# Kernel tuning notes

Measured on AMD Instinct MI355X. Metric: run time of the kernel, lower is better.

Reference implementation:

```python
import jax, jax.numpy as jnp
import numpy as np

B, L, C = 32, 1024, 32     # batch, seq_len, enc_in
D = 512                     # d_model / hidden_size
SEG = 16                    # seg_len
K = 25                      # moving_avg kernel
SX = L // SEG               # seg_num_x = 64 sequential GRU steps
PRED = 16                   # pred_len == seg_len -> seg_num_y = 1


def setup_inputs() -> dict:
    key = jax.random.key(0)
    ks = jax.random.split(key, 20)
    r = lambda i, shape: jax.random.normal(ks[i], shape, dtype=jnp.float32) * 0.05
    return {
        "x": jax.random.normal(ks[0], (B, L, C), dtype=jnp.float32),
        "W_emb": r(1, (D, SEG)), "b_emb": r(2, (D,)),
        "Wih_s": r(3, (3 * D, D)), "Whh_s": r(4, (3 * D, D)),
        "bih_s": r(5, (3 * D,)), "bhh_s": r(6, (3 * D,)),
        "Wih_t": r(7, (3 * D, D)), "Whh_t": r(8, (3 * D, D)),
        "bih_t": r(9, (3 * D,)), "bhh_t": r(10, (3 * D,)),
        "pos_s": r(11, (1, D // 2)), "ch_s": r(12, (C, D // 2)),
        "pos_t": r(13, (1, D // 2)), "ch_t": r(14, (C, D // 2)),
        "Wps": r(15, (SEG, D)), "bps": r(16, (SEG,)),
        "Wpt": r(17, (SEG, D)), "bpt": r(18, (SEG,)),
    }


def _moving_mean(x, k):
    # Autoformer moving_avg over dim 1 with edge replication (length preserved, k odd)
    pad = (k - 1) // 2
    xp = jnp.concatenate([jnp.repeat(x[:, :1], pad, 1), x, jnp.repeat(x[:, -1:], pad, 1)], axis=1)
    cs = jnp.cumsum(xp, axis=1)
    cs = jnp.concatenate([jnp.zeros_like(cs[:, :1]), cs], axis=1)
    return (cs[:, k:] - cs[:, :-k]) / k


def _gru_cell(x, h, Wih, Whh, bih, bhh):
    gi = x @ Wih.T + bih
    gh = h @ Whh.T + bhh
    ir, iz, in_ = jnp.split(gi, 3, axis=-1)
    hr, hz, hn = jnp.split(gh, 3, axis=-1)
    r = jax.nn.sigmoid(ir + hr)
    z = jax.nn.sigmoid(iz + hz)
    n = jnp.tanh(in_ + r * hn)
    return (1.0 - z) * n + z * h


def _forward(x, W_emb, b_emb, Wih_s, Whh_s, bih_s, bhh_s, Wih_t, Whh_t, bih_t, bhh_t,
             pos_s, ch_s, pos_t, ch_t, Wps, bps, Wpt, bpt):
    seq_last = jax.lax.stop_gradient(x[:, -1:, :])          # (B,1,C), detached
    xc = (x - seq_last).transpose(0, 2, 1)                  # (B,C,L)
    mean = _moving_mean(xc, K)                              # trend
    xs = xc - mean                                          # seasonal residual
    xt = mean
    # value embedding: (B*C, SX, SEG) -> (B*C, SX, D), ReLU
    xs = jax.nn.relu(xs.reshape(-1, SX, SEG) @ W_emb.T + b_emb)
    xt = jax.nn.relu(xt.reshape(-1, SX, SEG) @ W_emb.T + b_emb)
    N = B * C
    h0 = jnp.zeros((N, D), x.dtype)

    def step(carry, inp):
        hs, ht = carry
        xs_i, xt_i = inp
        hs = _gru_cell(xs_i, hs, Wih_s, Whh_s, bih_s, bhh_s)
        ht = _gru_cell(xt_i, ht, Wih_t, Whh_t, bih_t, bhh_t)
        return (hs, ht), None

    (hs, ht), _ = jax.lax.scan(step, (h0, h0), (xs.transpose(1, 0, 2), xt.transpose(1, 0, 2)))

    # decoder (seg_num_y == 1): pos/channel embedding -> one more GRUCell step
    pe_s = jnp.tile(jnp.concatenate([jnp.broadcast_to(pos_s, (C, D // 2)), ch_s], -1), (B, 1))  # (B*C,D)
    pe_t = jnp.tile(jnp.concatenate([jnp.broadcast_to(pos_t, (C, D // 2)), ch_t], -1), (B, 1))
    hs2 = _gru_cell(pe_s, hs, Wih_s, Whh_s, bih_s, bhh_s)
    ht2 = _gru_cell(pe_t, ht, Wih_t, Whh_t, bih_t, bhh_t)
    # predict heads (dropout is identity in eval)
    y = ht2 @ Wpt.T + bpt + hs2 @ Wps.T + bps               # (B*C, SEG)
    y = y.reshape(B, C, PRED).transpose(0, 2, 1)            # (B, PRED, C)
    return y + seq_last


def reference(x, W_emb, b_emb, Wih_s, Whh_s, bih_s, bhh_s, Wih_t, Whh_t, bih_t, bhh_t,
              pos_s, ch_s, pos_t, ch_t, Wps, bps, Wpt, bpt):
    return _forward(x, W_emb, b_emb, Wih_s, Whh_s, bih_s, bhh_s, Wih_t, Whh_t, bih_t, bhh_t,
                    pos_s, ch_s, pos_t, ch_t, Wps, bps, Wpt, bpt)
```

## Files before the change

kernel.cpp:

```cpp
#include <hip/hip_runtime.h>
#include <math.h>

#define B_   32
#define L_   1024
#define C_   32
#define D_   512
#define SEG_ 16
#define SX_  64
#define N_   1024

typedef _Float16 f16x8 __attribute__((ext_vector_type(8)));
typedef _Float16 f16x4 __attribute__((ext_vector_type(4)));
typedef float    f32x4 __attribute__((ext_vector_type(4)));

__device__ __forceinline__ void stage16(const void* g, void* l) {
    __builtin_amdgcn_global_load_lds((const __attribute__((address_space(1))) void*)g,
                                     (__attribute__((address_space(3))) void*)l, 16, 0, 0);
}
__device__ __forceinline__ void stage16l(const void* g, void* l) {
    __builtin_amdgcn_global_load_lds((const __attribute__((address_space(1))) void*)g,
                                     (__attribute__((address_space(3))) void*)l, 16, 0, 1);
}
__device__ __forceinline__ void store_v4_sc0(void* p, f16x8 v) {
    asm volatile("global_store_dwordx4 %0, %1, off sc0" :: "v"(p), "v"(v) : "memory");
}
__device__ __forceinline__ float fsig(float x) {
    return __builtin_amdgcn_rcpf(1.f + __expf(-x));
}
__device__ __forceinline__ float ftanh(float x) {
    return 1.f - 2.f * __builtin_amdgcn_rcpf(1.f + __expf(2.f * x));
}

__global__ __launch_bounds__(256) void prep_kernel(const float* __restrict__ x,
                                                   float* __restrict__ xs_seg,
                                                   float* __restrict__ xt_seg) {
    int b = blockIdx.x >> 2;
    int t = ((blockIdx.x & 3) << 8) + threadIdx.x;
    const float* xb    = x + (size_t)b * (L_ * C_);
    const float* xrow  = xb + (size_t)t * C_;
    const float* xlast = xb + (size_t)(L_ - 1) * C_;

    float diff[C_];
#pragma unroll
    for (int c = 0; c < C_; ++c) diff[c] = xrow[c] - xlast[c];
    float ps[C_ + 1];
    ps[0] = 0.f;
#pragma unroll
    for (int c = 0; c < C_; ++c) ps[c + 1] = ps[c] + diff[c];

    int s = t >> 4, q = t & 15;
#pragma unroll
    for (int c = 0; c < C_; ++c) {
        int lo = c - 12, hi = c + 12;
        float sum = ps[(hi < 31 ? hi : 31) + 1] - ps[lo > 0 ? lo : 0];
        if (lo < 0)  sum += (float)(-lo)     * diff[0];
        if (hi > 31) sum += (float)(hi - 31) * diff[31];
        float mean = sum * (1.0f / 25.0f);
        size_t idx = ((size_t)s * N_ + (size_t)(b * C_ + c)) * SEG_ + q;
        xt_seg[idx] = mean;
        xs_seg[idx] = diff[c] - mean;
    }
}

__global__ __launch_bounds__(256) void emb_kernel(
    const float* __restrict__ xs_seg, const float* __restrict__ xt_seg,
    const float* __restrict__ W_emb, const float* __restrict__ b_emb,
    _Float16* __restrict__ emb_buf, int s0) {
    int bid = blockIdx.x;
    int gru = bid >> 8, sl = (bid >> 4) & 15, nch = bid & 15;
    int step = s0 + sl, n0 = nch * 64;
    const float* xseg = gru ? xt_seg : xs_seg;
    __shared__ float xl[64 * 16];
    int tid = threadIdx.x;
    const float* src = xseg + ((size_t)step * N_ + n0) * SEG_;
    for (int i = tid; i < 1024; i += 256) xl[i] = src[i];

    int kg = tid & 127;
    int rh = tid >> 7;
    float w[4][16], bb[4];
#pragma unroll
    for (int i = 0; i < 4; ++i) {
        int k = kg * 4 + i;
        const float4* wr = (const float4*)(W_emb + (size_t)k * 16);
#pragma unroll
        for (int v = 0; v < 4; ++v) {
            float4 tt = wr[v];
            w[i][v * 4 + 0] = tt.x; w[i][v * 4 + 1] = tt.y;
            w[i][v * 4 + 2] = tt.z; w[i][v * 4 + 3] = tt.w;
        }
        bb[i] = b_emb[k];
    }
    __syncthreads();
    _Float16* dst = emb_buf + ((size_t)(sl * 2 + gru) * N_ + n0) * D_ + kg * 4;
    for (int r = 0; r < 32; ++r) {
        int row = rh * 32 + r;
        float a0 = bb[0], a1 = bb[1], a2 = bb[2], a3 = bb[3];
#pragma unroll
        for (int q = 0; q < 16; ++q) {
            float xv = xl[row * 16 + q];
            a0 = fmaf(xv, w[0][q], a0);
            a1 = fmaf(xv, w[1][q], a1);
            a2 = fmaf(xv, w[2][q], a2);
            a3 = fmaf(xv, w[3][q], a3);
        }
        f16x4 v;
        v[0] = (_Float16)(a0 > 0.f ? a0 : 0.f);
        v[1] = (_Float16)(a1 > 0.f ? a1 : 0.f);
        v[2] = (_Float16)(a2 > 0.f ? a2 : 0.f);
        v[3] = (_Float16)(a3 > 0.f ? a3 : 0.f);
        *(f16x4*)(dst + (size_t)row * D_) = v;
    }
}

__global__ __launch_bounds__(256) void pack_wih_kernel(
    const float* __restrict__ Wih_s, const float* __restrict__ Wih_t,
    _Float16* __restrict__ wp) {
    int e = blockIdx.x * 256 + threadIdx.x;
    int kk = e & 31;
    int t = e >> 5;
    int gc = t % 1536;
    int t2 = t / 1536;
    int kt = t2 & 15, gru = t2 >> 4;
    int member = gc / 192, r = gc % 192;
    int wn = r / 48, r2 = r % 48;
    int gate = r2 >> 4, jl = r2 & 15;
    int j = member * 64 + wn * 16 + jl;
    int k = kt * 32 + kk;
    const float* W = gru ? Wih_t : Wih_s;
    wp[e] = (_Float16)W[(size_t)(gate * 512 + j) * 512 + k];
}

__global__ __launch_bounds__(256) void pack_whh5_kernel(
    const float* __restrict__ Whh_s, const float* __restrict__ Whh_t,
    _Float16* __restrict__ wp) {
    int e = blockIdx.x * 256 + threadIdx.x;
    int fi = e & 7;
    int t = e >> 3;
    int c = t % 3072;
    int t2 = t / 3072;
    int kt = t2 & 3;
    int t3 = t2 >> 2;
    int member = t3 & 7, gru = t3 >> 3;
    int gc = c >> 4, s = c & 15;
    int q = s ^ (gc & 15);
    int k = kt * 128 + q * 8 + fi;
    int wn = gc / 48, r2 = gc % 48;
    int gate = r2 >> 4, jl = r2 & 15;
    int j = member * 64 + wn * 16 + jl;
    const float* W = gru ? Whh_t : Whh_s;
    wp[e] = (_Float16)W[(size_t)(gate * 512 + j) * 512 + k];
}

__global__ __launch_bounds__(256) void pack_pe_kernel(
    const float* __restrict__ pos_s, const float* __restrict__ ch_s,
    const float* __restrict__ pos_t, const float* __restrict__ ch_t,
    _Float16* __restrict__ pe) {
    int e = blockIdx.x * 256 + threadIdx.x;
    int k = e & 511;
    int n = (e >> 9) & 1023;
    int gru = e >> 19;
    int c = n & 31;
    const float* pos = gru ? pos_t : pos_s;
    const float* ch  = gru ? ch_t  : ch_s;
    float v = (k < 256) ? pos[k] : ch[c * 256 + (k - 256)];
    pe[e] = (_Float16)v;
}

__global__ __launch_bounds__(512, 2) void gi_gemm_kernel(
    const _Float16* __restrict__ emb, const _Float16* __restrict__ pe,
    const _Float16* __restrict__ wih_pack,
    _Float16* __restrict__ gi, _Float16* __restrict__ gi_pe, int mode) {
    __shared__ __align__(16) char smem[53248];
    char* sA = smem;
    char* sB = smem + 8192;
    int Mt = blockIdx.x & 7, Nt = blockIdx.x >> 3;
    int sl = blockIdx.y, gru = blockIdx.z;
    int tid = threadIdx.x, w = tid >> 6, lane = tid & 63;
    int wm = w & 1, wn = w >> 1, ml = lane & 15, qq = lane >> 4;

    const char* Ab = mode ? (const char*)(pe  + (size_t)gru * N_ * D_)
                          : (const char*)(emb + (size_t)(sl * 2 + gru) * N_ * D_);
    const char* Bb = (const char*)wih_pack + (size_t)gru * 16 * 1536 * 64
                     + (size_t)Nt * 192 * 64;

    int rA = tid >> 2, kqA = (tid & 3) ^ ((rA >> 1) & 3);
    const char* gA = Ab + (size_t)(Mt * 128 + rA) * 1024 + kqA * 16;
    int g1 = tid >> 2, kq1 = (tid & 3) ^ ((g1 >> 1) & 3);
    int c2 = 512 + tid, g2 = c2 >> 2, kq2 = (c2 & 3) ^ ((g2 >> 1) & 3);

    int offA[4], offB[3];
#pragma unroll
    for (int mf = 0; mf < 4; ++mf) {
        int row = wm * 64 + mf * 16 + ml;
        offA[mf] = (row * 4 + (qq ^ ((row >> 1) & 3))) * 16;
    }
#pragma unroll
    for (int g = 0; g < 3; ++g) {
        int gc = wn * 48 + g * 16 + ml;
        offB[g] = (gc * 4 + (qq ^ ((gc >> 1) & 3))) * 16;
    }

    f32x4 acc[4][3];
#pragma unroll
    for (int mf = 0; mf < 4; ++mf)
#pragma unroll
        for (int g = 0; g < 3; ++g) {
            f32x4 z = {0.f, 0.f, 0.f, 0.f};
            acc[mf][g] = z;
        }

    for (int kt = 0; kt < 16; ++kt) {
        __syncthreads();
        stage16(gA + kt * 64, sA + w * 1024);
        const char* Bkt = Bb + (size_t)kt * (1536 * 64);
        stage16(Bkt + g1 * 64 + kq1 * 16, sB + w * 1024);
        if (w < 4) stage16(Bkt + g2 * 64 + kq2 * 16, sB + 8192 + w * 1024);
        asm volatile("s_waitcnt vmcnt(0)" ::: "memory");
        __syncthreads();
        f16x8 a[4];
#pragma unroll
        for (int mf = 0; mf < 4; ++mf) a[mf] = *(const f16x8*)(sA + offA[mf]);
#pragma unroll
        for (int g = 0; g < 3; ++g) {
            f16x8 b = *(const f16x8*)(sB + offB[g]);
#pragma unroll
            for (int mf = 0; mf < 4; ++mf)
                acc[mf][g] = __builtin_amdgcn_mfma_f32_16x16x32_f16(a[mf], b, acc[mf][g], 0, 0, 0);
        }
    }

    __syncthreads();
#pragma unroll
    for (int mf = 0; mf < 4; ++mf) {
        int wm_c = mf >> 1, rt = mf & 1;
        int tid_c = (wn * 2 + wm_c) * 64 + qq * 16 + ml;
        char* base = smem + wm * 26624 + tid_c * 52;
#pragma unroll
        for (int g = 0; g < 3; ++g)
#pragma unroll
            for (int reg = 0; reg < 4; ++reg) {
                int v = rt * 12 + reg * 3 + g;
                *(_Float16*)(base + v * 2) = (_Float16)acc[mf][g][reg];
            }
    }
    __syncthreads();
    _Float16* ob = mode ? gi_pe + (size_t)gru * 8 * 16 * 512 * 24
                        : gi    + (size_t)(sl * 2 + gru) * 8 * 16 * 512 * 24;
    char* obB = (char*)ob;
#pragma unroll
    for (int s = 0; s < 6; ++s) {
        int o = tid * 16 + s * 8192;
        int mc = o / 24576;
        int o2 = o - mc * 24576;
        int tc = o2 / 48;
        int r  = o2 - tc * 48;
        const char* src = smem + mc * 26624 + tc * 52 + r;
        int4 val;
        val.x = *(const int*)(src);
        val.y = *(const int*)(src + 4);
        val.z = *(const int*)(src + 8);
        val.w = *(const int*)(src + 12);
        *(int4*)(obB + (size_t)(Nt * 16 + Mt * 2 + mc) * 24576 + o2) = val;
    }
}

__global__ __launch_bounds__(512) void gru_chain_kernel(
    const _Float16* __restrict__ whh_pk5,
    const _Float16* __restrict__ gi_base,
    const float* __restrict__ bih_s, const float* __restrict__ bhh_s,
    const float* __restrict__ bih_t, const float* __restrict__ bhh_t,
    _Float16* __restrict__ hbf0, _Float16* __restrict__ hbf1,
    unsigned* __restrict__ flags, int nsteps, int sbase) {
    __shared__ __align__(16) char sA[65536];
    __shared__ __align__(16) char sEx[49152];
    int bid = blockIdx.x;
    int member = bid >> 5, chain = bid & 31;
    int Mt = chain & 15, gru = chain >> 4;
    int tid = threadIdx.x, w = tid >> 6, lane = tid & 63;
    int ml = lane & 15, qq = lane >> 4;
    int km = w & 1, wn = w >> 1;

    const char* h0 = (const char*)hbf0 + ((size_t)gru * N_ + Mt * 64) * 1024;
    const char* h1 = (const char*)hbf1 + ((size_t)gru * N_ + Mt * 64) * 1024;

    f16x8 bfr[3][8];
    {
        const _Float16* Wb = whh_pk5 + (size_t)(gru * 8 + member) * 4 * 24576;
#pragma unroll
        for (int g = 0; g < 3; ++g) {
            int gc = wn * 48 + g * 16 + ml;
#pragma unroll
            for (int ks = 0; ks < 8; ++ks) {
                int kt = km * 2 + (ks >> 2);
                int q8 = ((ks & 3) * 4 + qq) ^ (gc & 15);
                bfr[g][ks] = *(const f16x8*)(Wb + (size_t)kt * 24576
                                             + (size_t)(gc * 16 + q8) * 8);
            }
        }
    }

    int cS0 = (lane & 48) | ((lane & 15) ^ (w & 15));
    int cS1 = (lane & 48) | ((lane & 15) ^ ((w + 8) & 15));

    int offR[4], cp[8];
#pragma unroll
    for (int rt = 0; rt < 4; ++rt) offR[rt] = (rt * 16 + ml) * 1024;
#pragma unroll
    for (int ks = 0; ks < 8; ++ks) {
        int c = km * 32 + ks * 4 + qq;
        cp[ks] = ((c & 48) | ((c & 15) ^ ml)) * 16;
    }

    const float* bi = gru ? bih_t : bih_s;
    const float* bh = gru ? bhh_t : bhh_s;
    int j = member * 64 + wn * 16 + ml;
    float bir = bi[j], biz = bi[D_ + j], bin = bi[2 * D_ + j];
    float bhr = bh[j], bhz = bh[D_ + j], bhn = bh[2 * D_ + j];
    float hp[2][4];
#pragma unroll
    for (int rtL = 0; rtL < 2; ++rtL)
#pragma unroll
        for (int reg = 0; reg < 4; ++reg) {
            int row = Mt * 64 + km * 32 + rtL * 16 + qq * 4 + reg;
            hp[rtL][reg] = (float)hbf0[((size_t)gru * N_ + row) * D_ + j];
        }

    unsigned* fbase = flags + chain * 256;
    const _Float16* giTid0 = gi_base
        + (((size_t)gru * 8 + member) * 16 + Mt) * 512 * 24 + (size_t)tid * 24;
    size_t giStep = (size_t)2 * 8 * 16 * 512 * 24;

    int dir0 = sbase & 1;
    f16x8 gv0, gv1, gv2;
    {
        const _Float16* gp = giTid0;
        gv0 = *(const f16x8*)(gp);
        gv1 = *(const f16x8*)(gp + 8);
        gv2 = *(const f16x8*)(gp + 16);
        const char* hin = dir0 ? h1 : h0;
#pragma unroll
        for (int r = 0; r < 8; ++r) {
            int row = r * 8 + w;
            stage16l(hin + (size_t)row * 1024 + (size_t)((r & 1) ? cS1 : cS0) * 16,
                     sA + row * 1024);
        }
    }

    for (int it = 0; it < nsteps; ++it) {
        int gstep = sbase + it;
        _Float16* hout = (gstep & 1) ? hbf0 : hbf1;

        f32x4 acc[4][3];
#pragma unroll
        for (int rt = 0; rt < 4; ++rt)
#pragma unroll
            for (int g = 0; g < 3; ++g) {
                f32x4 z = {0.f, 0.f, 0.f, 0.f};
                acc[rt][g] = z;
            }

        asm volatile("s_waitcnt vmcnt(0)" ::: "memory");
        __syncthreads();

        int itn = (it + 1 < nsteps) ? it + 1 : it;
        const _Float16* gpn = giTid0 + (size_t)itn * giStep;
        f16x8 ngv0 = *(const f16x8*)(gpn);
        f16x8 ngv1 = *(const f16x8*)(gpn + 8);
        f16x8 ngv2 = *(const f16x8*)(gpn + 16);
        __builtin_amdgcn_sched_barrier(0);

#pragma unroll
        for (int ks = 0; ks < 8; ++ks) {
            f16x8 a0 = *(const f16x8*)(sA + offR[0] + cp[ks]);
            f16x8 a1 = *(const f16x8*)(sA + offR[1] + cp[ks]);
            f16x8 a2 = *(const f16x8*)(sA + offR[2] + cp[ks]);
            f16x8 a3 = *(const f16x8*)(sA + offR[3] + cp[ks]);
#pragma unroll
            for (int g = 0; g < 3; ++g) {
                acc[0][g] = __builtin_amdgcn_mfma_f32_16x16x32_f16(a0, bfr[g][ks], acc[0][g], 0, 0, 0);
                acc[1][g] = __builtin_amdgcn_mfma_f32_16x16x32_f16(a1, bfr[g][ks], acc[1][g], 0, 0, 0);
                acc[2][g] = __builtin_amdgcn_mfma_f32_16x16x32_f16(a2, bfr[g][ks], acc[2][g], 0, 0, 0);
                acc[3][g] = __builtin_amdgcn_mfma_f32_16x16x32_f16(a3, bfr[g][ks], acc[3][g], 0, 0, 0);
            }
        }

        char* exw = sEx + (size_t)(wn * 64 + lane) * 16;
        if (km == 0) {
#pragma unroll
            for (int g = 0; g < 3; ++g) {
                *(f32x4*)(exw + (size_t)(6 + g) * 4096) = acc[2][g];
                *(f32x4*)(exw + (size_t)(9 + g) * 4096) = acc[3][g];
            }
        } else {
#pragma unroll
            for (int g = 0; g < 3; ++g) {
                *(f32x4*)(exw + (size_t)(0 + g) * 4096) = acc[0][g];
                *(f32x4*)(exw + (size_t)(3 + g) * 4096) = acc[1][g];
            }
        }
        __syncthreads();
        f32x4 s0[3], s1[3];
        if (km == 0) {
#pragma unroll
            for (int g = 0; g < 3; ++g) {
                s0[g] = acc[0][g] + *(const f32x4*)(exw + (size_t)(0 + g) * 4096);
                s1[g] = acc[1][g] + *(const f32x4*)(exw + (size_t)(3 + g) * 4096);
            }
        } else {
#pragma unroll
            for (int g = 0; g < 3; ++g) {
                s0[g] = acc[2][g] + *(const f32x4*)(exw + (size_t)(6 + g) * 4096);
                s1[g] = acc[3][g] + *(const f32x4*)(exw + (size_t)(9 + g) * 4096);
            }
        }

        char* sH = sA;
        int colb = (wn * 16 + ml) * 2;
#pragma unroll
        for (int reg = 0; reg < 4; ++reg) {
            int v0 = reg * 3;
            float gr = (float)((v0 + 0) < 8 ? gv0[(v0 + 0) & 7]
                      : ((v0 + 0) < 16 ? gv1[(v0 + 0) & 7] : gv2[(v0 + 0) & 7]));
            float gz = (float)((v0 + 1) < 8 ? gv0[(v0 + 1) & 7]
                      : ((v0 + 1) < 16 ? gv1[(v0 + 1) & 7] : gv2[(v0 + 1) & 7]));
            float gn = (float)((v0 + 2) < 8 ? gv0[(v0 + 2) & 7]
                      : ((v0 + 2) < 16 ? gv1[(v0 + 2) & 7] : gv2[(v0 + 2) & 7]));
            float r = fsig(s0[0][reg] + gr + bir + bhr);
            float z = fsig(s0[1][reg] + gz + biz + bhz);
            float nn = ftanh(gn + bin + r * (s0[2][reg] + bhn));
            float hv = (1.f - z) * nn + z * hp[0][reg];
            hp[0][reg] = hv;
            int rl = km * 32 + qq * 4 + reg;
            *(_Float16*)(sH + rl * 144 + colb) = (_Float16)hv;
        }
#pragma unroll
        for (int reg = 0; reg < 4; ++reg) {
            int v0 = 12 + reg * 3;
            float gr = (float)((v0 + 0) < 8 ? gv0[(v0 + 0) & 7]
                      : ((v0 + 0) < 16 ? gv1[(v0 + 0) & 7] : gv2[(v0 + 0) & 7]));
            float gz = (float)((v0 + 1) < 8 ? gv0[(v0 + 1) & 7]
                      : ((v0 + 1) < 16 ? gv1[(v0 + 1) & 7] : gv2[(v0 + 1) & 7]));
            float gn = (float)((v0 + 2) < 8 ? gv0[(v0 + 2) & 7]
                      : ((v0 + 2) < 16 ? gv1[(v0 + 2) & 7] : gv2[(v0 + 2) & 7]));
            float r = fsig(s1[0][reg] + gr + bir + bhr);
            float z = fsig(s1[1][reg] + gz + biz + bhz);
            float nn = ftanh(gn + bin + r * (s1[2][reg] + bhn));
            float hv = (1.f - z) * nn + z * hp[1][reg];
            hp[1][reg] = hv;
            int rl = km * 32 + 16 + qq * 4 + reg;
            *(_Float16*)(sH + rl * 144 + colb) = (_Float16)hv;
        }
        __syncthreads();
        {
            int srow = tid >> 3, spart = tid & 7;
            f16x8 hv8 = *(const f16x8*)(sH + srow * 144 + spart * 16);
            _Float16* gdst = hout + ((size_t)gru * N_ + Mt * 64 + srow) * D_
                             + member * 64 + spart * 8;
            store_v4_sc0(gdst, hv8);
        }

        asm volatile("s_waitcnt vmcnt(0)" ::: "memory");
        __syncthreads();
        if (tid == 0)
            __hip_atomic_store(fbase + member * 32, (unsigned)(gstep + 1),
                               __ATOMIC_RELAXED, __HIP_MEMORY_SCOPE_AGENT);

        if (it < nsteps - 1) {
            if (w == 0) {
                const unsigned* fp = fbase + (lane & 7) * 32;
                unsigned tgt = (unsigned)(gstep + 1);
                int guard = 0;
                while (true) {
                    unsigned v = __hip_atomic_load(fp, __ATOMIC_RELAXED,
                                                   __HIP_MEMORY_SCOPE_AGENT);
                    if (__all(v >= tgt)) break;
                    __builtin_amdgcn_s_sleep(1);
                    if (++guard > (1 << 20)) break;
                }
            }
            __syncthreads();
            const char* hinN = ((gstep + 1) & 1) ? h1 : h0;
#pragma unroll
            for (int r = 0; r < 8; ++r) {
                int row = r * 8 + w;
                stage16l(hinN + (size_t)row * 1024 + (size_t)((r & 1) ? cS1 : cS0) * 16,
                         sA + row * 1024);
            }
        }
        gv0 = ngv0; gv1 = ngv1; gv2 = ngv2;
    }
}

__global__ __launch_bounds__(256) void head_kernel(
    const _Float16* __restrict__ hs2, const _Float16* __restrict__ ht2,
    const float* __restrict__ Wps, const float* __restrict__ bps,
    const float* __restrict__ Wpt, const float* __restrict__ bpt,
    const float* __restrict__ x, float* __restrict__ out) {
    int g = blockIdx.x * 256 + threadIdx.x;
    int n = g >> 4, p = g & 15;
    int b = n >> 5, c = n & 31;
    const _Float16* hs = hs2 + (size_t)n * D_;
    const _Float16* ht = ht2 + (size_t)n * D_;
    const float* ws = Wps + (size_t)p * D_;
    const float* wt = Wpt + (size_t)p * D_;
    float acc = bps[p] + bpt[p];
    for (int k = 0; k < D_; ++k)
        acc += (float)hs[k] * ws[k] + (float)ht[k] * wt[k];
    float last = x[((size_t)b * L_ + (L_ - 1)) * C_ + c];
    out[((size_t)b * SEG_ + p) * C_ + c] = acc + last;
}

extern "C" void kernel_launch(void* const* d_in, const int* in_sizes, int n_in,
                              void* d_out, int out_size, void* d_ws, size_t ws_size,
                              hipStream_t stream) {
    const float* x     = (const float*)d_in[0];
    const float* W_emb = (const float*)d_in[1];
    const float* b_emb = (const float*)d_in[2];
    const float* Wih_s = (const float*)d_in[3];
    const float* Whh_s = (const float*)d_in[4];
    const float* bih_s = (const float*)d_in[5];
    const float* bhh_s = (const float*)d_in[6];
    const float* Wih_t = (const float*)d_in[7];
    const float* Whh_t = (const float*)d_in[8];
    const float* bih_t = (const float*)d_in[9];
    const float* bhh_t = (const float*)d_in[10];
    const float* pos_s = (const float*)d_in[11];
    const float* ch_s  = (const float*)d_in[12];
    const float* pos_t = (const float*)d_in[13];
    const float* ch_t  = (const float*)d_in[14];
    const float* Wps   = (const float*)d_in[15];
    const float* bps   = (const float*)d_in[16];
    const float* Wpt   = (const float*)d_in[17];
    const float* bpt   = (const float*)d_in[18];
    float* out = (float*)d_out;

    const size_t SZ_XS    = (size_t)SX_ * N_ * SEG_ * 4;
    const size_t SZ_EMB   = (size_t)16 * 2 * N_ * D_ * 2;
    const size_t SZ_GIB   = (size_t)16 * 2 * 8 * 16 * 512 * 24 * 2;
    const size_t SZ_GIPE  = (size_t)2 * 8 * 16 * 512 * 24 * 2;
    const size_t SZ_PE    = (size_t)2 * N_ * D_ * 2;
    const size_t SZ_WIH   = (size_t)2 * 16 * 1536 * 32 * 2;
    const size_t SZ_WHH   = (size_t)2 * 8 * 4 * 3072 * 8 * 2;
    const size_t SZ_H     = (size_t)2 * N_ * D_ * 2;
    const size_t SZ_FLAGS = 32 * 256 * 4;
    const size_t fixed = 2 * SZ_XS + SZ_EMB + SZ_GIPE + SZ_PE + SZ_WIH + SZ_WHH
                         + 2 * SZ_H + SZ_FLAGS;
    const bool big = ws_size >= fixed + 4 * SZ_GIB;
    const size_t gi_bytes = big ? 4 * SZ_GIB : SZ_GIB;

    char* p = (char*)d_ws;
    float* xs_seg = (float*)p;          p += SZ_XS;
    float* xt_seg = (float*)p;          p += SZ_XS;
    _Float16* emb_buf = (_Float16*)p;   p += SZ_EMB;
    _Float16* gi_buf  = (_Float16*)p;   p += gi_bytes;
    _Float16* gi_pe   = (_Float16*)p;   p += SZ_GIPE;
    _Float16* pe_buf  = (_Float16*)p;   p += SZ_PE;
    _Float16* wih_pk  = (_Float16*)p;   p += SZ_WIH;
    _Float16* whh_pk5 = (_Float16*)p;   p += SZ_WHH;
    _Float16* hbf0 = (_Float16*)p;      p += SZ_H;
    _Float16* hbf1 = (_Float16*)p;      p += SZ_H;
    unsigned* flags = (unsigned*)p;     p += SZ_FLAGS;

    hipMemsetAsync(hbf0, 0, SZ_H, stream);
    hipMemsetAsync(flags, 0, SZ_FLAGS, stream);

    pack_wih_kernel<<<6144, 256, 0, stream>>>(Wih_s, Wih_t, wih_pk);
    pack_whh5_kernel<<<6144, 256, 0, stream>>>(Whh_s, Whh_t, whh_pk5);
    pack_pe_kernel<<<4096, 256, 0, stream>>>(pos_s, ch_s, pos_t, ch_t, pe_buf);
    prep_kernel<<<B_ * 4, 256, 0, stream>>>(x, xs_seg, xt_seg);

    const size_t giBatchElems = (size_t)16 * 2 * 8 * 16 * 512 * 24;
    if (big) {
        for (int b = 0; b < 4; ++b) {
            emb_kernel<<<512, 256, 0, stream>>>(xs_seg, xt_seg, W_emb, b_emb,
                                                emb_buf, b * 16);
            gi_gemm_kernel<<<dim3(64, 16, 2), 512, 0, stream>>>(
                emb_buf, pe_buf, wih_pk, gi_buf + (size_t)b * giBatchElems, gi_pe, 0);
        }
        gru_chain_kernel<<<256, 512, 0, stream>>>(
            whh_pk5, gi_buf, bih_s, bhh_s, bih_t, bhh_t,
            hbf0, hbf1, flags, 64, 0);
    } else {
        for (int b = 0; b < 4; ++b) {
            emb_kernel<<<512, 256, 0, stream>>>(xs_seg, xt_seg, W_emb, b_emb,
                                                emb_buf, b * 16);
            gi_gemm_kernel<<<dim3(64, 16, 2), 512, 0, stream>>>(
                emb_buf, pe_buf, wih_pk, gi_buf, gi_pe, 0);
            gru_chain_kernel<<<256, 512, 0, stream>>>(
                whh_pk5, gi_buf, bih_s, bhh_s, bih_t, bhh_t,
                hbf0, hbf1, flags, 16, b * 16);
        }
    }
    gi_gemm_kernel<<<dim3(64, 1, 2), 512, 0, stream>>>(
        emb_buf, pe_buf, wih_pk, gi_buf, gi_pe, 1);
    gru_chain_kernel<<<256, 512, 0, stream>>>(
        whh_pk5, gi_pe, bih_s, bhh_s, bih_t, bhh_t,
        hbf0, hbf1, flags, 1, 64);

    head_kernel<<<N_ * SEG_ / 256, 256, 0, stream>>>(
        hbf1, hbf1 + (size_t)N_ * D_, Wps, bps, Wpt, bpt, x, out);
}
```

Before: 773.3 us.

## Overlap GRU recurrence chain with next batch's input-gate GEMM in fused kernel

Wraps the GI GEMM and the GRU chain in device functions and adds a fused kernel. Its first 256 blocks run the recurrent chain for the current 16-step batch, and the remaining blocks compute the input-gate GEMM for the next batch into a double-buffered gi area. The GEMM work thereby fills the CUs left idle by the 256-block latency-bound chain. It also shrinks chain shared memory by sharing one 64KB buffer and adds a syncthreads before exchange writes. The risk is that GEMM blocks may compete with the chain's spin-waiting persistent blocks for CUs or bandwidth, or delay the chain blocks' residency and create scheduling hazards.

```diff
diff --git a/kernel.cpp b/kernel.cpp
--- a/kernel.cpp
+++ b/kernel.cpp
@@ -166,15 +166,14 @@
     pe[e] = (_Float16)v;
 }
 
-__global__ __launch_bounds__(512, 2) void gi_gemm_kernel(
+__device__ __forceinline__ void gemm_body(
     const _Float16* __restrict__ emb, const _Float16* __restrict__ pe,
     const _Float16* __restrict__ wih_pack,
-    _Float16* __restrict__ gi, _Float16* __restrict__ gi_pe, int mode) {
-    __shared__ __align__(16) char smem[53248];
+    _Float16* __restrict__ gi, _Float16* __restrict__ gi_pe, int mode,
+    int xb, int sl, int gru, char* smem) {
     char* sA = smem;
     char* sB = smem + 8192;
-    int Mt = blockIdx.x & 7, Nt = blockIdx.x >> 3;
-    int sl = blockIdx.y, gru = blockIdx.z;
+    int Mt = xb & 7, Nt = xb >> 3;
     int tid = threadIdx.x, w = tid >> 6, lane = tid & 63;
     int wm = w & 1, wn = w >> 1, ml = lane & 15, qq = lane >> 4;
 
@@ -264,16 +263,23 @@
     }
 }
 
-__global__ __launch_bounds__(512) void gru_chain_kernel(
-    const _Float16* __restrict__ whh_pk5,
-    const _Float16* __restrict__ gi_base,
+__global__ __launch_bounds__(512, 2) void gi_gemm_kernel(
+    const _Float16* __restrict__ emb, const _Float16* __restrict__ pe,
+    const _Float16* __restrict__ wih_pack,
+    _Float16* __restrict__ gi, _Float16* __restrict__ gi_pe, int mode) {
+    __shared__ __align__(16) char smem[53248];
+    gemm_body(emb, pe, wih_pack, gi, gi_pe, mode,
+              blockIdx.x, blockIdx.y, blockIdx.z, smem);
+}
+
+__device__ __forceinline__ void chain_body(
+    const _Float16* __restrict__ whh_pk5, const _Float16* __restrict__ gi_base,
     const float* __restrict__ bih_s, const float* __restrict__ bhh_s,
     const float* __restrict__ bih_t, const float* __restrict__ bhh_t,
     _Float16* __restrict__ hbf0, _Float16* __restrict__ hbf1,
-    unsigned* __restrict__ flags, int nsteps, int sbase) {
-    __shared__ __align__(16) char sA[65536];
-    __shared__ __align__(16) char sEx[49152];
-    int bid = blockIdx.x;
+    unsigned* __restrict__ flags, int nsteps, int sbase, int bid, char* smem) {
+    char* sA = smem;
+    char* sEx = smem + 16384;
     int member = bid >> 5, chain = bid & 31;
     int Mt = chain & 15, gru = chain >> 4;
     int tid = threadIdx.x, w = tid >> 6, lane = tid & 63;
@@ -384,6 +390,7 @@
             }
         }
 
+        __syncthreads();
         char* exw = sEx + (size_t)(wn * 64 + lane) * 16;
         if (km == 0) {
 #pragma unroll
@@ -488,6 +495,37 @@
             }
         }
         gv0 = ngv0; gv1 = ngv1; gv2 = ngv2;
+    }
+}
+
+__global__ __launch_bounds__(512) void gru_chain_kernel(
+    const _Float16* __restrict__ whh_pk5, const _Float16* __restrict__ gi_base,
+    const float* __restrict__ bih_s, const float* __restrict__ bhh_s,
+    const float* __restrict__ bih_t, const float* __restrict__ bhh_t,
+    _Float16* __restrict__ hbf0, _Float16* __restrict__ hbf1,
+    unsigned* __restrict__ flags, int nsteps, int sbase) {
+    __shared__ __align__(16) char smem[65536];
+    chain_body(whh_pk5, gi_base, bih_s, bhh_s, bih_t, bhh_t,
+               hbf0, hbf1, flags, nsteps, sbase, blockIdx.x, smem);
+}
+
+__global__ __launch_bounds__(512, 2) void fused_kernel(
+    const _Float16* __restrict__ whh_pk5, const _Float16* __restrict__ gi_rd,
+    const float* __restrict__ bih_s, const float* __restrict__ bhh_s,
+    const float* __restrict__ bih_t, const float* __restrict__ bhh_t,
+    _Float16* __restrict__ hbf0, _Float16* __restrict__ hbf1,
+    unsigned* __restrict__ flags, int nsteps, int sbase,
+    const _Float16* __restrict__ emb, const _Float16* __restrict__ pe,
+    const _Float16* __restrict__ wih_pack, _Float16* __restrict__ gi_wr) {
+    __shared__ __align__(16) char smem[65536];
+    int bid = blockIdx.x;
+    if (bid < 256) {
+        chain_body(whh_pk5, gi_rd, bih_s, bhh_s, bih_t, bhh_t,
+                   hbf0, hbf1, flags, nsteps, sbase, bid, smem);
+    } else {
+        int b2 = bid - 256;
+        int xb = b2 & 63, sl = (b2 >> 6) & 15, gru = b2 >> 10;
+        gemm_body(emb, pe, wih_pack, gi_wr, (_Float16*)0, 0, xb, sl, gru, smem);
     }
 }
 
@@ -545,8 +583,8 @@
     const size_t SZ_FLAGS = 32 * 256 * 4;
     const size_t fixed = 2 * SZ_XS + SZ_EMB + SZ_GIPE + SZ_PE + SZ_WIH + SZ_WHH
                          + 2 * SZ_H + SZ_FLAGS;
-    const bool big = ws_size >= fixed + 4 * SZ_GIB;
-    const size_t gi_bytes = big ? 4 * SZ_GIB : SZ_GIB;
+    const bool overlap = ws_size >= fixed + 2 * SZ_GIB;
+    const size_t gi_bytes = overlap ? 2 * SZ_GIB : SZ_GIB;
 
     char* p = (char*)d_ws;
     float* xs_seg = (float*)p;          p += SZ_XS;
@@ -569,17 +607,23 @@
     pack_pe_kernel<<<4096, 256, 0, stream>>>(pos_s, ch_s, pos_t, ch_t, pe_buf);
     prep_kernel<<<B_ * 4, 256, 0, stream>>>(x, xs_seg, xt_seg);
 
-    const size_t giBatchElems = (size_t)16 * 2 * 8 * 16 * 512 * 24;
-    if (big) {
-        for (int b = 0; b < 4; ++b) {
+    const size_t giHalfElems = (size_t)16 * 2 * 8 * 16 * 512 * 24;
+    if (overlap) {
+        _Float16* giH[2] = { gi_buf, gi_buf + giHalfElems };
+        emb_kernel<<<512, 256, 0, stream>>>(xs_seg, xt_seg, W_emb, b_emb, emb_buf, 0);
+        gi_gemm_kernel<<<dim3(64, 16, 2), 512, 0, stream>>>(
+            emb_buf, pe_buf, wih_pk, giH[0], gi_pe, 0);
+        for (int b = 0; b < 3; ++b) {
             emb_kernel<<<512, 256, 0, stream>>>(xs_seg, xt_seg, W_emb, b_emb,
-                                                emb_buf, b * 16);
-            gi_gemm_kernel<<<dim3(64, 16, 2), 512, 0, stream>>>(
-                emb_buf, pe_buf, wih_pk, gi_buf + (size_t)b * giBatchElems, gi_pe, 0);
+                                                emb_buf, (b + 1) * 16);
+            fused_kernel<<<2304, 512, 0, stream>>>(
+                whh_pk5, giH[b & 1], bih_s, bhh_s, bih_t, bhh_t,
+                hbf0, hbf1, flags, 16, b * 16,
+                emb_buf, pe_buf, wih_pk, giH[(b + 1) & 1]);
         }
         gru_chain_kernel<<<256, 512, 0, stream>>>(
-            whh_pk5, gi_buf, bih_s, bhh_s, bih_t, bhh_t,
-            hbf0, hbf1, flags, 64, 0);
+            whh_pk5, giH[1], bih_s, bhh_s, bih_t, bhh_t,
+            hbf0, hbf1, flags, 16, 48);
     } else {
         for (int b = 0; b < 4; ++b) {
             emb_kernel<<<512, 256, 0, stream>>>(xs_seg, xt_seg, W_emb, b_emb,
```

After: 859.6 us. +11.2%, slower.

## Merge setup kernels and split GRU chain into two halves with a smaller gi buffer

Applied to the files above, without the earlier changes.

Four preprocessing kernels (two weight packs, the positional-embedding pack and the decomposition prep) become one setup_kernel launch that branches on block index. The gate-input buffer now holds two 16-step batches instead of four. The recurrent chain runs as two launches: 32 steps, then 33 steps, with the decoder step folded into the second launch. That fold relies on gi_pe sitting directly after gi_buf in the workspace, so step 64 reads the decoder gate inputs. The aim is to cut launch count and shrink the gi working set so it is more likely to stay in cache, at the cost of an extra chain launch and serialising the second-half GEMMs behind the first chain.

```diff
diff --git a/kernel.cpp b/kernel.cpp
--- a/kernel.cpp
+++ b/kernel.cpp
@@ -31,34 +31,83 @@
     return 1.f - 2.f * __builtin_amdgcn_rcpf(1.f + __expf(2.f * x));
 }
 
-__global__ __launch_bounds__(256) void prep_kernel(const float* __restrict__ x,
-                                                   float* __restrict__ xs_seg,
-                                                   float* __restrict__ xt_seg) {
-    int b = blockIdx.x >> 2;
-    int t = ((blockIdx.x & 3) << 8) + threadIdx.x;
-    const float* xb    = x + (size_t)b * (L_ * C_);
-    const float* xrow  = xb + (size_t)t * C_;
-    const float* xlast = xb + (size_t)(L_ - 1) * C_;
-
-    float diff[C_];
-#pragma unroll
-    for (int c = 0; c < C_; ++c) diff[c] = xrow[c] - xlast[c];
-    float ps[C_ + 1];
-    ps[0] = 0.f;
-#pragma unroll
-    for (int c = 0; c < C_; ++c) ps[c + 1] = ps[c] + diff[c];
-
-    int s = t >> 4, q = t & 15;
-#pragma unroll
-    for (int c = 0; c < C_; ++c) {
-        int lo = c - 12, hi = c + 12;
-        float sum = ps[(hi < 31 ? hi : 31) + 1] - ps[lo > 0 ? lo : 0];
-        if (lo < 0)  sum += (float)(-lo)     * diff[0];
-        if (hi > 31) sum += (float)(hi - 31) * diff[31];
-        float mean = sum * (1.0f / 25.0f);
-        size_t idx = ((size_t)s * N_ + (size_t)(b * C_ + c)) * SEG_ + q;
-        xt_seg[idx] = mean;
-        xs_seg[idx] = diff[c] - mean;
+__global__ __launch_bounds__(256) void setup_kernel(
+    const float* __restrict__ x, float* __restrict__ xs_seg, float* __restrict__ xt_seg,
+    const float* __restrict__ Wih_s, const float* __restrict__ Wih_t,
+    _Float16* __restrict__ wih_pk,
+    const float* __restrict__ Whh_s, const float* __restrict__ Whh_t,
+    _Float16* __restrict__ whh_pk5,
+    const float* __restrict__ pos_s, const float* __restrict__ ch_s,
+    const float* __restrict__ pos_t, const float* __restrict__ ch_t,
+    _Float16* __restrict__ pe) {
+    int bid = blockIdx.x, tid = threadIdx.x;
+    if (bid < 6144) {
+        int e = bid * 256 + tid;
+        int kk = e & 31;
+        int t = e >> 5;
+        int gc = t % 1536;
+        int t2 = t / 1536;
+        int kt = t2 & 15, gru = t2 >> 4;
+        int member = gc / 192, r = gc % 192;
+        int wn = r / 48, r2 = r % 48;
+        int gate = r2 >> 4, jl = r2 & 15;
+        int j = member * 64 + wn * 16 + jl;
+        int k = kt * 32 + kk;
+        const float* W = gru ? Wih_t : Wih_s;
+        wih_pk[e] = (_Float16)W[(size_t)(gate * 512 + j) * 512 + k];
+    } else if (bid < 12288) {
+        int e = (bid - 6144) * 256 + tid;
+        int fi = e & 7;
+        int t = e >> 3;
+        int c = t % 3072;
+        int t2 = t / 3072;
+        int kt = t2 & 3;
+        int t3 = t2 >> 2;
+        int member = t3 & 7, gru = t3 >> 3;
+        int gc = c >> 4, s = c & 15;
+        int q = s ^ (gc & 15);
+        int k = kt * 128 + q * 8 + fi;
+        int wn = gc / 48, r2 = gc % 48;
+        int gate = r2 >> 4, jl = r2 & 15;
+        int j = member * 64 + wn * 16 + jl;
+        const float* W = gru ? Whh_t : Whh_s;
+        whh_pk5[e] = (_Float16)W[(size_t)(gate * 512 + j) * 512 + k];
+    } else if (bid < 16384) {
+        int e = (bid - 12288) * 256 + tid;
+        int k = e & 511;
+        int n = (e >> 9) & 1023;
+        int gru = e >> 19;
+        int c = n & 31;
+        const float* pos = gru ? pos_t : pos_s;
+        const float* ch  = gru ? ch_t  : ch_s;
+        float v = (k < 256) ? pos[k] : ch[c * 256 + (k - 256)];
+        pe[e] = (_Float16)v;
+    } else {
+        int b2 = bid - 16384;
+        int b = b2 >> 2;
+        int t = ((b2 & 3) << 8) + tid;
+        const float* xb    = x + (size_t)b * (L_ * C_);
+        const float* xrow  = xb + (size_t)t * C_;
+        const float* xlast = xb + (size_t)(L_ - 1) * C_;
+        float diff[C_];
+#pragma unroll
+        for (int c = 0; c < C_; ++c) diff[c] = xrow[c] - xlast[c];
+        float ps[C_ + 1];
+        ps[0] = 0.f;
+#pragma unroll
+        for (int c = 0; c < C_; ++c) ps[c + 1] = ps[c] + diff[c];
+        int s = t >> 4, q = t & 15;
+#pragma unroll
+        for (int c = 0; c < C_; ++c) {
+            int lo = c - 12, hi = c + 12;
+            float sum = ps[(hi < 31 ? hi : 31) + 1] - ps[lo > 0 ? lo : 0];
+            if (lo < 0)  sum += (float)(-lo)     * diff[0];
+            if (hi > 31) sum += (float)(hi - 31) * diff[31];
+            float mean = sum * (1.0f / 25.0f);
+            size_t idx = ((size_t)s * N_ + (size_t)(b * C_ + c)) * SEG_ + q;
+            xt_seg[idx] = mean;
+            xs_seg[idx] = diff[c] - mean;
+        }
     }
 }
 
@@ -110,60 +159,6 @@
         v[3] = (_Float16)(a3 > 0.f ? a3 : 0.f);
         *(f16x4*)(dst + (size_t)row * D_) = v;
     }
-}
-
-__global__ __launch_bounds__(256) void pack_wih_kernel(
-    const float* __restrict__ Wih_s, const float* __restrict__ Wih_t,
-    _Float16* __restrict__ wp) {
-    int e = blockIdx.x * 256 + threadIdx.x;
-    int kk = e & 31;
-    int t = e >> 5;
-    int gc = t % 1536;
-    int t2 = t / 1536;
-    int kt = t2 & 15, gru = t2 >> 4;
-    int member = gc / 192, r = gc % 192;
-    int wn = r / 48, r2 = r % 48;
-    int gate = r2 >> 4, jl = r2 & 15;
-    int j = member * 64 + wn * 16 + jl;
-    int k = kt * 32 + kk;
-    const float* W = gru ? Wih_t : Wih_s;
-    wp[e] = (_Float16)W[(size_t)(gate * 512 + j) * 512 + k];
-}
-
-__global__ __launch_bounds__(256) void pack_whh5_kernel(
-    const float* __restrict__ Whh_s, const float* __restrict__ Whh_t,
-    _Float16* __restrict__ wp) {
-    int e = blockIdx.x * 256 + threadIdx.x;
-    int fi = e & 7;
-    int t = e >> 3;
-    int c = t % 3072;
-    int t2 = t / 3072;
-    int kt = t2 & 3;
-    int t3 = t2 >> 2;
-    int member = t3 & 7, gru = t3 >> 3;
-    int gc = c >> 4, s = c & 15;
-    int q = s ^ (gc & 15);
-    int k = kt * 128 + q * 8 + fi;
-    int wn = gc / 48, r2 = gc % 48;
-    int gate = r2 >> 4, jl = r2 & 15;
-    int j = member * 64 + wn * 16 + jl;
-    const float* W = gru ? Whh_t : Whh_s;
-    wp[e] = (_Float16)W[(size_t)(gate * 512 + j) * 512 + k];
-}
-
-__global__ __launch_bounds__(256) void pack_pe_kernel(
-    const float* __restrict__ pos_s, const float* __restrict__ ch_s,
-    const float* __restrict__ pos_t, const float* __restrict__ ch_t,
-    _Float16* __restrict__ pe) {
-    int e = blockIdx.x * 256 + threadIdx.x;
-    int k = e & 511;
-    int n = (e >> 9) & 1023;
-    int gru = e >> 19;
-    int c = n & 31;
-    const float* pos = gru ? pos_t : pos_s;
-    const float* ch  = gru ? ch_t  : ch_s;
-    float v = (k < 256) ? pos[k] : ch[c * 256 + (k - 256)];
-    pe[e] = (_Float16)v;
 }
 
 __global__ __launch_bounds__(512, 2) void gi_gemm_kernel(
@@ -545,8 +540,8 @@
     const size_t SZ_FLAGS = 32 * 256 * 4;
     const size_t fixed = 2 * SZ_XS + SZ_EMB + SZ_GIPE + SZ_PE + SZ_WIH + SZ_WHH
                          + 2 * SZ_H + SZ_FLAGS;
-    const bool big = ws_size >= fixed + 4 * SZ_GIB;
-    const size_t gi_bytes = big ? 4 * SZ_GIB : SZ_GIB;
+    const bool big2 = ws_size >= fixed + 2 * SZ_GIB;
+    const size_t gi_bytes = big2 ? 2 * SZ_GIB : SZ_GIB;
 
     char* p = (char*)d_ws;
     float* xs_seg = (float*)p;          p += SZ_XS;
@@ -564,14 +559,13 @@
     hipMemsetAsync(hbf0, 0, SZ_H, stream);
     hipMemsetAsync(flags, 0, SZ_FLAGS, stream);
 
-    pack_wih_kernel<<<6144, 256, 0, stream>>>(Wih_s, Wih_t, wih_pk);
-    pack_whh5_kernel<<<6144, 256, 0, stream>>>(Whh_s, Whh_t, whh_pk5);
-    pack_pe_kernel<<<4096, 256, 0, stream>>>(pos_s, ch_s, pos_t, ch_t, pe_buf);
-    prep_kernel<<<B_ * 4, 256, 0, stream>>>(x, xs_seg, xt_seg);
+    setup_kernel<<<16512, 256, 0, stream>>>(
+        x, xs_seg, xt_seg, Wih_s, Wih_t, wih_pk, Whh_s, Whh_t, whh_pk5,
+        pos_s, ch_s, pos_t, ch_t, pe_buf);
 
     const size_t giBatchElems = (size_t)16 * 2 * 8 * 16 * 512 * 24;
-    if (big) {
-        for (int b = 0; b < 4; ++b) {
+    if (big2) {
+        for (int b = 0; b < 2; ++b) {
             emb_kernel<<<512, 256, 0, stream>>>(xs_seg, xt_seg, W_emb, b_emb,
                                                 emb_buf, b * 16);
             gi_gemm_kernel<<<dim3(64, 16, 2), 512, 0, stream>>>(
@@ -579,7 +573,19 @@
         }
         gru_chain_kernel<<<256, 512, 0, stream>>>(
             whh_pk5, gi_buf, bih_s, bhh_s, bih_t, bhh_t,
-            hbf0, hbf1, flags, 64, 0);
+            hbf0, hbf1, flags, 32, 0);
+        for (int b = 2; b < 4; ++b) {
+            emb_kernel<<<512, 256, 0, stream>>>(xs_seg, xt_seg, W_emb, b_emb,
+                                                emb_buf, b * 16);
+            gi_gemm_kernel<<<dim3(64, 16, 2), 512, 0, stream>>>(
+                emb_buf, pe_buf, wih_pk, gi_buf + (size_t)(b - 2) * giBatchElems,
+                gi_pe, 0);
+        }
+        gi_gemm_kernel<<<dim3(64, 1, 2), 512, 0, stream>>>(
+            emb_buf, pe_buf, wih_pk, gi_buf, gi_pe, 1);
+        gru_chain_kernel<<<256, 512, 0, stream>>>(
+            whh_pk5, gi_buf, bih_s, bhh_s, bih_t, bhh_t,
+            hbf0, hbf1, flags, 33, 32);
     } else {
         for (int b = 0; b < 4; ++b) {
             emb_kernel<<<512, 256, 0, stream>>>(xs_seg, xt_seg, W_emb, b_emb,
@@ -590,12 +596,12 @@
                 whh_pk5, gi_buf, bih_s, bhh_s, bih_t, bhh_t,
                 hbf0, hbf1, flags, 16, b * 16);
         }
-    }
-    gi_gemm_kernel<<<dim3(64, 1, 2), 512, 0, stream>>>(
-        emb_buf, pe_buf, wih_pk, gi_buf, gi_pe, 1);
-    gru_chain_kernel<<<256, 512, 0, stream>>>(
-        whh_pk5, gi_pe, bih_s, bhh_s, bih_t, bhh_t,
-        hbf0, hbf1, flags, 1, 64);
+        gi_gemm_kernel<<<dim3(64, 1, 2), 512, 0, stream>>>(
+            emb_buf, pe_buf, wih_pk, gi_buf, gi_pe, 1);
+        gru_chain_kernel<<<256, 512, 0, stream>>>(
+            whh_pk5, gi_pe, bih_s, bhh_s, bih_t, bhh_t,
+            hbf0, hbf1, flags, 1, 64);
+    }
 
     head_kernel<<<N_ * SEG_ / 256, 256, 0, stream>>>(
         hbf1, hbf1 + (size_t)N_ * D_, Wps, bps, Wpt, bpt, x, out);
```

Result: faster. 751.8 us (-2.8%).
